# Kernel tuning notes

Hardware: AMD Instinct MI355X
Metric: run time of the kernel (lower is better)

Reference implementation:

```python
import jax, jax.numpy as jnp
import numpy as np

BETA = 30.0


def setup_inputs() -> dict:
    key = jax.random.key(0)
    k_x, k1, k2, k3, kv = jax.random.split(key, 5)
    B, D = 4096, 128
    N = 32  # nodes per hidden layer
    VALUE_SCALE = 500.0
    return {
        "x": jax.random.normal(k_x, (B, D), dtype=jnp.float32),
        "W1": jax.random.normal(k1, (N, D), dtype=jnp.float32),
        "W2": jax.random.normal(k2, (N, D), dtype=jnp.float32),
        "W3": jax.random.normal(k3, (N, D), dtype=jnp.float32),
        "V": jax.random.normal(kv, (1, N, N, N), dtype=jnp.float32) / VALUE_SCALE,
    }


def reference(x, W1, W2, W3, V):
    # feat='sf': every gating layer reads the raw input x (h is never updated).
    # gate_i = sigmoid(beta * x @ W_i^T), shape [B, 32]
    g1 = jax.nn.sigmoid(BETA * (x @ W1.T))
    g2 = jax.nn.sigmoid(BETA * (x @ W2.T))
    g3 = jax.nn.sigmoid(BETA * (x @ W3.T))
    # prod='op': cp[b,i,j,k] = g1[b,i]*g2[b,j]*g3[b,k];
    # out[b] = sum_{ijk} cp[b,i,j,k] * V[0,i,j,k]  -- expressed as one contraction.
    return jnp.einsum("bi,bj,bk,ijk->b", g1, g2, g3, V[0])
```

## Files before the change

kernel.cpp:

```cpp
#include <hip/hip_runtime.h>


#define BETA 30.0f

__device__ __forceinline__ float f4c(const float4 v, int c) {
    return c == 0 ? v.x : (c == 1 ? v.y : (c == 2 ? v.z : v.w));
}

__device__ __forceinline__ float qp_xor1(float a) {
    return __int_as_float(__builtin_amdgcn_mov_dpp(__float_as_int(a), 0xB1, 0xF, 0xF, true));
}
__device__ __forceinline__ float qp_xor2(float a) {
    return __int_as_float(__builtin_amdgcn_mov_dpp(__float_as_int(a), 0x4E, 0xF, 0xF, true));
}

__global__ __launch_bounds__(256, 2) void dlgn_v12_kernel(
    const float* __restrict__ x,
    const float* __restrict__ W1,
    const float* __restrict__ W2,
    const float* __restrict__ W3,
    const float* __restrict__ V,
    float* __restrict__ out)
{
    __shared__ float xlds[8 * 160];
    __shared__ float Gs[8][100];
    __shared__ float Plds[2560];

    const int t  = threadIdx.x;
    const int b0 = blockIdx.x * 8;

    {
        const int r    = t >> 5;
        const int col4 = t & 31;
        const float4 xv = ((const float4*)(x + (size_t)(b0 + r) * 128))[col4];
        const int skc = col4 >> 2, sc = col4 & 3;
        *(float4*)&xlds[r * 160 + skc * 20 + sc * 4] = xv;
    }

    const int fl = t >> 3;
    const int kc = t & 7;
    float4 w1c[4], w2c[4], w3c[4];
    {
        const float4* W1r = (const float4*)(W1 + fl * 128 + kc * 16);
        const float4* W2r = (const float4*)(W2 + fl * 128 + kc * 16);
        const float4* W3r = (const float4*)(W3 + fl * 128 + kc * 16);
#pragma unroll
        for (int c = 0; c < 4; ++c) {
            w1c[c] = W1r[c]; w2c[c] = W2r[c]; w3c[c] = W3r[c];
        }
    }
    __syncthreads();

    float acc[3][8];
#pragma unroll
    for (int m = 0; m < 3; ++m)
#pragma unroll
        for (int r = 0; r < 8; ++r) acc[m][r] = 0.f;

#pragma unroll
    for (int r = 0; r < 8; ++r) {
        float4 xc[4];
#pragma unroll
        for (int c = 0; c < 4; ++c)
            xc[c] = *(const float4*)&xlds[r * 160 + kc * 20 + c * 4];
#pragma unroll
        for (int c = 0; c < 4; ++c) {
            acc[0][r] = fmaf(w1c[c].x, xc[c].x, acc[0][r]);
            acc[0][r] = fmaf(w1c[c].y, xc[c].y, acc[0][r]);
            acc[0][r] = fmaf(w1c[c].z, xc[c].z, acc[0][r]);
            acc[0][r] = fmaf(w1c[c].w, xc[c].w, acc[0][r]);
            acc[1][r] = fmaf(w2c[c].x, xc[c].x, acc[1][r]);
            acc[1][r] = fmaf(w2c[c].y, xc[c].y, acc[1][r]);
            acc[1][r] = fmaf(w2c[c].z, xc[c].z, acc[1][r]);
            acc[1][r] = fmaf(w2c[c].w, xc[c].w, acc[1][r]);
            acc[2][r] = fmaf(w3c[c].x, xc[c].x, acc[2][r]);
            acc[2][r] = fmaf(w3c[c].y, xc[c].y, acc[2][r]);
            acc[2][r] = fmaf(w3c[c].z, xc[c].z, acc[2][r]);
            acc[2][r] = fmaf(w3c[c].w, xc[c].w, acc[2][r]);
        }
    }

    const float4* V4 = (const float4*)V;
    float4 v[32];
#pragma unroll
    for (int i = 0; i < 32; ++i) v[i] = V4[i * 256 + t];

#pragma unroll
    for (int m = 0; m < 3; ++m) {
        float sel = 0.f;
#pragma unroll
        for (int r = 0; r < 8; ++r) {
            float a = acc[m][r];
            a += qp_xor1(a);
            a += qp_xor2(a);
            a += __shfl_xor(a, 4);
            if (kc == r) sel = a;
        }
        Gs[kc][32 * m + fl] = 1.0f / (1.0f + __expf(-BETA * sel));
    }
    __syncthreads();

    const int j  = t >> 3;
    const int c2 = t & 7;

    float p8[8];
#pragma unroll
    for (int b = 0; b < 8; ++b) {
        const float  ga  = Gs[b][t & 31];
        const float  g2s = Gs[b][32 + j];
        const float4 g3r = *(const float4*)&Gs[b][64 + c2 * 4];

        float ux = 0.f, uy = 0.f, uz = 0.f, uw = 0.f;
#pragma unroll
        for (int i = 0; i < 32; ++i) {
            const float g1i = __int_as_float(
                __builtin_amdgcn_readlane(__float_as_int(ga), i));
            ux = fmaf(g1i, v[i].x, ux);
            uy = fmaf(g1i, v[i].y, uy);
            uz = fmaf(g1i, v[i].z, uz);
            uw = fmaf(g1i, v[i].w, uw);
        }
        float s = ux * g3r.x;
        s = fmaf(uy, g3r.y, s);
        s = fmaf(uz, g3r.z, s);
        s = fmaf(uw, g3r.w, s);
        p8[b] = s * g2s;
    }

    *(float4*)&Plds[t * 10]     = make_float4(p8[0], p8[1], p8[2], p8[3]);
    *(float4*)&Plds[t * 10 + 4] = make_float4(p8[4], p8[5], p8[6], p8[7]);
    __syncthreads();

    {
        const int fb2 = t >> 5;
        const int pt  = t & 31;
        float s = 0.f;
#pragma unroll
        for (int s8 = 0; s8 < 8; ++s8)
            s += Plds[(pt + s8 * 32) * 10 + fb2];
        s += __shfl_xor(s, 1);
        s += __shfl_xor(s, 2);
        s += __shfl_xor(s, 4);
        s += __shfl_xor(s, 8);
        s += __shfl_xor(s, 16);
        if (pt == 0) out[b0 + fb2] = s;
    }
}

extern "C" void kernel_launch(void* const* d_in, const int* in_sizes, int n_in,
                              void* d_out, int out_size, void* d_ws, size_t ws_size,
                              hipStream_t stream) {
    const float* x  = (const float*)d_in[0];
    const float* W1 = (const float*)d_in[1];
    const float* W2 = (const float*)d_in[2];
    const float* W3 = (const float*)d_in[3];
    const float* V  = (const float*)d_in[4];
    float* out = (float*)d_out;

    dlgn_v12_kernel<<<dim3(512), dim3(256), 0, stream>>>(x, W1, W2, W3, V, out);
}
```

Before: 13.97 us.

## Double block size to 512 threads, splitting batch rows and V i-range across halves

Doubles threads per block to 512, with two halves of 256 threads. In the gate phase each half handles 4 of the 8 batch rows. In the V-contraction phase each half handles 16 of the 32 i indices, halving per-thread V registers (from 32 float4 to 16). Partial sums from both halves are combined in a larger shared-memory reduction with a wider shuffle. The aim is more wave-level parallelism and lower register pressure per thread, at the cost of redundantly loading W in both halves and a bigger final reduction.

```diff
diff --git a/kernel.cpp b/kernel.cpp
--- a/kernel.cpp
+++ b/kernel.cpp
@@ -2,10 +2,6 @@
 
 
 #define BETA 30.0f
-
-__device__ __forceinline__ float f4c(const float4 v, int c) {
-    return c == 0 ? v.x : (c == 1 ? v.y : (c == 2 ? v.z : v.w));
-}
 
 __device__ __forceinline__ float qp_xor1(float a) {
     return __int_as_float(__builtin_amdgcn_mov_dpp(__float_as_int(a), 0xB1, 0xF, 0xF, true));
@@ -14,7 +10,7 @@
     return __int_as_float(__builtin_amdgcn_mov_dpp(__float_as_int(a), 0x4E, 0xF, 0xF, true));
 }
 
-__global__ __launch_bounds__(256, 2) void dlgn_v12_kernel(
+__global__ __launch_bounds__(512, 4) void dlgn_v13_kernel(
     const float* __restrict__ x,
     const float* __restrict__ W1,
     const float* __restrict__ W2,
@@ -24,12 +20,14 @@
 {
     __shared__ float xlds[8 * 160];
     __shared__ float Gs[8][100];
-    __shared__ float Plds[2560];
+    __shared__ float Plds[512 * 10];
 
     const int t  = threadIdx.x;
+    const int ih = t >> 8;
+    const int tl = t & 255;
     const int b0 = blockIdx.x * 8;
 
-    {
+    if (t < 256) {
         const int r    = t >> 5;
         const int col4 = t & 31;
         const float4 xv = ((const float4*)(x + (size_t)(b0 + r) * 128))[col4];
@@ -37,8 +35,8 @@
         *(float4*)&xlds[r * 160 + skc * 20 + sc * 4] = xv;
     }
 
-    const int fl = t >> 3;
-    const int kc = t & 7;
+    const int fl = tl >> 3;
+    const int kc = tl & 7;
     float4 w1c[4], w2c[4], w3c[4];
     {
         const float4* W1r = (const float4*)(W1 + fl * 128 + kc * 16);
@@ -51,57 +49,60 @@
     }
     __syncthreads();
 
-    float acc[3][8];
+    float acc[3][4];
 #pragma unroll
     for (int m = 0; m < 3; ++m)
 #pragma unroll
-        for (int r = 0; r < 8; ++r) acc[m][r] = 0.f;
+        for (int rr = 0; rr < 4; ++rr) acc[m][rr] = 0.f;
 
 #pragma unroll
-    for (int r = 0; r < 8; ++r) {
+    for (int rr = 0; rr < 4; ++rr) {
+        const int row = ih * 4 + rr;
         float4 xc[4];
 #pragma unroll
         for (int c = 0; c < 4; ++c)
-            xc[c] = *(const float4*)&xlds[r * 160 + kc * 20 + c * 4];
+            xc[c] = *(const float4*)&xlds[row * 160 + kc * 20 + c * 4];
 #pragma unroll
         for (int c = 0; c < 4; ++c) {
-            acc[0][r] = fmaf(w1c[c].x, xc[c].x, acc[0][r]);
-            acc[0][r] = fmaf(w1c[c].y, xc[c].y, acc[0][r]);
-            acc[0][r] = fmaf(w1c[c].z, xc[c].z, acc[0][r]);
-            acc[0][r] = fmaf(w1c[c].w, xc[c].w, acc[0][r]);
-            acc[1][r] = fmaf(w2c[c].x, xc[c].x, acc[1][r]);
-            acc[1][r] = fmaf(w2c[c].y, xc[c].y, acc[1][r]);
-            acc[1][r] = fmaf(w2c[c].z, xc[c].z, acc[1][r]);
-            acc[1][r] = fmaf(w2c[c].w, xc[c].w, acc[1][r]);
-            acc[2][r] = fmaf(w3c[c].x, xc[c].x, acc[2][r]);
-            acc[2][r] = fmaf(w3c[c].y, xc[c].y, acc[2][r]);
-            acc[2][r] = fmaf(w3c[c].z, xc[c].z, acc[2][r]);
-            acc[2][r] = fmaf(w3c[c].w, xc[c].w, acc[2][r]);
+            acc[0][rr] = fmaf(w1c[c].x, xc[c].x, acc[0][rr]);
+            acc[0][rr] = fmaf(w1c[c].y, xc[c].y, acc[0][rr]);
+            acc[0][rr] = fmaf(w1c[c].z, xc[c].z, acc[0][rr]);
+            acc[0][rr] = fmaf(w1c[c].w, xc[c].w, acc[0][rr]);
+            acc[1][rr] = fmaf(w2c[c].x, xc[c].x, acc[1][rr]);
+            acc[1][rr] = fmaf(w2c[c].y, xc[c].y, acc[1][rr]);
+            acc[1][rr] = fmaf(w2c[c].z, xc[c].z, acc[1][rr]);
+            acc[1][rr] = fmaf(w2c[c].w, xc[c].w, acc[1][rr]);
+            acc[2][rr] = fmaf(w3c[c].x, xc[c].x, acc[2][rr]);
+            acc[2][rr] = fmaf(w3c[c].y, xc[c].y, acc[2][rr]);
+            acc[2][rr] = fmaf(w3c[c].z, xc[c].z, acc[2][rr]);
+            acc[2][rr] = fmaf(w3c[c].w, xc[c].w, acc[2][rr]);
         }
     }
 
     const float4* V4 = (const float4*)V;
-    float4 v[32];
+    float4 v[16];
 #pragma unroll
-    for (int i = 0; i < 32; ++i) v[i] = V4[i * 256 + t];
+    for (int il = 0; il < 16; ++il)
+        v[il] = V4[(ih * 16 + il) * 256 + tl];
 
 #pragma unroll
     for (int m = 0; m < 3; ++m) {
         float sel = 0.f;
 #pragma unroll
-        for (int r = 0; r < 8; ++r) {
-            float a = acc[m][r];
+        for (int rr = 0; rr < 4; ++rr) {
+            float a = acc[m][rr];
             a += qp_xor1(a);
             a += qp_xor2(a);
             a += __shfl_xor(a, 4);
-            if (kc == r) sel = a;
+            if (kc == rr) sel = a;
         }
-        Gs[kc][32 * m + fl] = 1.0f / (1.0f + __expf(-BETA * sel));
+        if (kc < 4)
+            Gs[ih * 4 + kc][32 * m + fl] = 1.0f / (1.0f + __expf(-BETA * sel));
     }
     __syncthreads();
 
-    const int j  = t >> 3;
-    const int c2 = t & 7;
+    const int j  = tl >> 3;
+    const int c2 = tl & 7;
 
     float p8[8];
 #pragma unroll
@@ -112,13 +113,13 @@
 
         float ux = 0.f, uy = 0.f, uz = 0.f, uw = 0.f;
 #pragma unroll
-        for (int i = 0; i < 32; ++i) {
+        for (int il = 0; il < 16; ++il) {
             const float g1i = __int_as_float(
-                __builtin_amdgcn_readlane(__float_as_int(ga), i));
-            ux = fmaf(g1i, v[i].x, ux);
-            uy = fmaf(g1i, v[i].y, uy);
-            uz = fmaf(g1i, v[i].z, uz);
-            uw = fmaf(g1i, v[i].w, uw);
+                __builtin_amdgcn_readlane(__float_as_int(ga), ih * 16 + il));
+            ux = fmaf(g1i, v[il].x, ux);
+            uy = fmaf(g1i, v[il].y, uy);
+            uz = fmaf(g1i, v[il].z, uz);
+            uw = fmaf(g1i, v[il].w, uw);
         }
         float s = ux * g3r.x;
         s = fmaf(uy, g3r.y, s);
@@ -132,17 +133,18 @@
     __syncthreads();
 
     {
-        const int fb2 = t >> 5;
-        const int pt  = t & 31;
+        const int fb2 = t >> 6;
+        const int pt  = t & 63;
         float s = 0.f;
 #pragma unroll
         for (int s8 = 0; s8 < 8; ++s8)
-            s += Plds[(pt + s8 * 32) * 10 + fb2];
+            s += Plds[(pt + s8 * 64) * 10 + fb2];
         s += __shfl_xor(s, 1);
         s += __shfl_xor(s, 2);
         s += __shfl_xor(s, 4);
         s += __shfl_xor(s, 8);
         s += __shfl_xor(s, 16);
+        s += __shfl_xor(s, 32);
         if (pt == 0) out[b0 + fb2] = s;
     }
 }
@@ -157,5 +159,5 @@
     const float* V  = (const float*)d_in[4];
     float* out = (float*)d_out;
 
-    dlgn_v12_kernel<<<dim3(512), dim3(256), 0, stream>>>(x, W1, W2, W3, V, out);
+    dlgn_v13_kernel<<<dim3(512), dim3(512), 0, stream>>>(x, W1, W2, W3, V, out);
 }
```

Measured after the change: 30.97 us. +121.8%, slower.
